# Kernel optimization log

Measured on AMD Instinct MI355X. Metric: run time of the kernel, lower is better.

The kernel has to match this reference:

```python
import jax, jax.numpy as jnp
import numpy as np

EPS = 1e-5
SLOPE = 0.2


def _bn(x, g, b, m, v):
    # eval-mode BatchNorm1d over channel dim (last axis here)
    return (x - m) * (g * jax.lax.rsqrt(v + EPS)) + b


def _lrelu(x):
    return jnp.where(x >= 0, x, SLOPE * x)


def setup_inputs() -> dict:
    key = jax.random.key(0)
    ks = jax.random.split(key, 24)
    B, N = 16, 2048
    d = {
        "x_query": jax.random.normal(ks[0], (B, 2048), jnp.float32),
        "x_key": jax.random.normal(ks[1], (B, N, 512), jnp.float32),
        "W1": jax.random.normal(ks[2], (2048, 512), jnp.float32) * 0.02,
        "W2": jax.random.normal(ks[3], (512, 2048), jnp.float32) * 0.02,
        "W3": jax.random.normal(ks[4], (64, 512), jnp.float32) * 0.02,
        "W4": jax.random.normal(ks[5], (1, 64), jnp.float32) * 0.02,
    }
    for i, c in zip(range(4), (2048, 512, 64, 1)):
        d[f"g{i+1}"] = jax.random.uniform(ks[6 + 4 * i], (c,), jnp.float32, 0.5, 1.5)
        d[f"b{i+1}"] = jax.random.normal(ks[7 + 4 * i], (c,), jnp.float32) * 0.1
        d[f"m{i+1}"] = jax.random.normal(ks[8 + 4 * i], (c,), jnp.float32) * 0.1
        d[f"v{i+1}"] = jax.random.uniform(ks[9 + 4 * i], (c,), jnp.float32, 0.5, 1.5)
    return d


def reference(x_query, x_key, W1, W2, W3, W4,
              g1, b1, m1, v1, g2, b2, m2, v2,
              g3, b3, m3, v3, g4, b4, m4, v4):
    # values: [B, N, 2048]
    values = _lrelu(_bn(jnp.einsum('bnd,ed->bne', x_key, W1), g1, b1, m1, v1))
    features = values + x_query[:, None, :]
    s = _lrelu(_bn(jnp.einsum('bne,de->bnd', features, W2), g2, b2, m2, v2))
    s = _lrelu(_bn(jnp.einsum('bnd,kd->bnk', s, W3), g3, b3, m3, v3))
    s = _lrelu(_bn(jnp.einsum('bnk,ok->bno', s, W4), g4, b4, m4, v4))  # [B,N,1]
    scores = jax.nn.softmax(s[..., 0], axis=1)  # [B,N]
    feature = jnp.einsum('bne,bn->be', values, scores)  # softmax-weighted sum pool
    return feature
```

## Files before the change

### kernel.cpp

```cpp
#include <hip/hip_runtime.h>
#include <hip/hip_bf16.h>

typedef __bf16 bf16x8 __attribute__((ext_vector_type(8)));
typedef float f32x4 __attribute__((ext_vector_type(4)));
typedef __attribute__((address_space(3))) void lds_void_t;
typedef __attribute__((address_space(1))) void gbl_void_t;

#define LRELU(x) ((x) >= 0.f ? (x) : 0.2f * (x))

__device__ __forceinline__ void gload16(void* lds_uniform, const void* gsrc) {
    __builtin_amdgcn_global_load_lds((const gbl_void_t*)gsrc, (lds_void_t*)lds_uniform,
                                     16, 0, 0);
}

__device__ __forceinline__ unsigned short f2u(float f) {
    __hip_bfloat16 h = __float2bfloat16(f);
    return reinterpret_cast<unsigned short&>(h);
}

__global__ void cvt_f32_bf16(const float* __restrict__ in,
                             __hip_bfloat16* __restrict__ out, int n4) {
    int stride = gridDim.x * blockDim.x;
    for (int i = blockIdx.x * blockDim.x + threadIdx.x; i < n4; i += stride) {
        float4 v = reinterpret_cast<const float4*>(in)[i];
        ushort4 o;
        o.x = f2u(v.x); o.y = f2u(v.y); o.z = f2u(v.z); o.w = f2u(v.w);
        reinterpret_cast<ushort4*>(out)[i] = o;
    }
}

template <int N, int K, int MODE>
__global__ __launch_bounds__(512, 2)
void gemm256(const __hip_bfloat16* __restrict__ A,
             const __hip_bfloat16* __restrict__ Bw,
             const float* __restrict__ xq,
             __hip_bfloat16* __restrict__ out,
             const float* __restrict__ Gg, const float* __restrict__ Gb,
             const float* __restrict__ Gm, const float* __restrict__ Gv) {
    __shared__ __hip_bfloat16 sm[3 * 16384];

    const int nwg = gridDim.x;
    const int cpx = nwg >> 3;
    const int bid = blockIdx.x;
    const int orig = (bid & 7) * cpx + (bid >> 3);
    constexpr int NCB = N / 256;
    const int rowblk = orig / NCB;
    const int colblk = orig % NCB;
    const int row0 = rowblk * 256, col0 = colblk * 256;

    const int tid = threadIdx.x;
    const int lane = tid & 63;
    const int wv = tid >> 6;
    const int wm = wv >> 2, wn = wv & 3;
    const int lr = lane & 15, kg = lane >> 4;

    const int srow = tid >> 2;
    const int sc = tid & 3;
    const int kch = ((sc ^ ((srow >> 1) & 3)) << 3);
    const __hip_bfloat16* As0 = A + (size_t)(row0 + srow) * K + kch;
    const __hip_bfloat16* As1 = A + (size_t)(row0 + 128 + srow) * K + kch;
    const __hip_bfloat16* Bs0 = Bw + (size_t)(col0 + srow) * K + kch;
    const __hip_bfloat16* Bs1 = Bw + (size_t)(col0 + 128 + srow) * K + kch;

    auto STAGE_A = [&](int b, int k0) {
        __hip_bfloat16* la = sm + b * 16384 + wv * 512;
        gload16(la,        As0 + k0);
        gload16(la + 4096, As1 + k0);
    };
    auto STAGE_B = [&](int b, int k0) {
        __hip_bfloat16* lb = sm + b * 16384 + 8192 + wv * 512;
        gload16(lb,        Bs0 + k0);
        gload16(lb + 4096, Bs1 + k0);
    };

    const int f = (lr >> 1) & 3;
    const int koff = ((kg ^ f) << 3);
    const int aoff = (wm * 128 + lr) * 32 + koff;
    const int boff = 8192 + (wn * 64 + lr) * 32 + koff;

    f32x4 acc[8][4];
#pragma unroll
    for (int i = 0; i < 8; ++i)
#pragma unroll
        for (int j = 0; j < 4; ++j) acc[i][j] = (f32x4){0.f, 0.f, 0.f, 0.f};

    constexpr int nt = K / 32;
    STAGE_A(0, 0);  STAGE_B(0, 0);
    STAGE_A(1, 32); STAGE_B(1, 32);

    for (int t = 0; t < nt; ++t) {
        if (t + 1 < nt) {
            asm volatile("s_waitcnt vmcnt(4)" ::: "memory");
        } else {
            asm volatile("s_waitcnt vmcnt(0)" ::: "memory");
        }
        __builtin_amdgcn_s_barrier();
        __builtin_amdgcn_sched_barrier(0);

        const __hip_bfloat16* base = sm + (t % 3) * 16384;
        bf16x8 af[8], bfr[4];

        if (t + 2 < nt) {
            STAGE_A((t + 2) % 3, (t + 2) * 32);
            STAGE_B((t + 2) % 3, (t + 2) * 32);
        }
#pragma unroll
        for (int i = 0; i < 8; ++i)
            af[i] = *reinterpret_cast<const bf16x8*>(base + aoff + i * 512);
#pragma unroll
        for (int j = 0; j < 4; ++j)
            bfr[j] = *reinterpret_cast<const bf16x8*>(base + boff + j * 512);

#pragma unroll
        for (int i = 0; i < 8; ++i)
#pragma unroll
            for (int j = 0; j < 4; ++j)
                acc[i][j] = __builtin_amdgcn_mfma_f32_16x16x32_bf16(af[i], bfr[j], acc[i][j], 0, 0, 0);
    }

    const int bq = row0 >> 11;
    float scl[4], tcn[4], xqv[4];
#pragma unroll
    for (int j = 0; j < 4; ++j) {
        const int c = col0 + wn * 64 + j * 16 + lr;
        scl[j] = Gg[c] * rsqrtf(Gv[c] + 1e-5f);
        tcn[j] = Gb[c] - Gm[c] * scl[j];
        xqv[j] = (MODE == 1) ? xq[bq * 2048 + c] : 0.f;
    }
#pragma unroll
    for (int i = 0; i < 8; ++i) {
#pragma unroll
        for (int rI = 0; rI < 4; ++rI) {
            const int r = row0 + wm * 128 + i * 16 + kg * 4 + rI;
            const size_t rowoff = (size_t)r * N + col0 + wn * 64 + lr;
#pragma unroll
            for (int j = 0; j < 4; ++j) {
                float val = acc[i][j][rI] * scl[j] + tcn[j];
                val = LRELU(val) + xqv[j];
                out[rowoff + j * 16] = __float2bfloat16(val);
            }
        }
    }
}

__global__ __launch_bounds__(256)
void gemm3_l4(const __hip_bfloat16* __restrict__ A,
              const __hip_bfloat16* __restrict__ W3b,
              const float* __restrict__ W4,
              const float* __restrict__ g3, const float* __restrict__ b3,
              const float* __restrict__ m3, const float* __restrict__ v3,
              const float* __restrict__ g4, const float* __restrict__ b4,
              const float* __restrict__ m4, const float* __restrict__ v4,
              float* __restrict__ logits) {
    const int lane = threadIdx.x & 63;
    const int wv = threadIdx.x >> 6;
    const int row0 = blockIdx.x * 128 + wv * 32;
    const int lr = lane & 15, kg = lane >> 4;

    f32x4 acc[2][4];
#pragma unroll
    for (int i = 0; i < 2; ++i)
#pragma unroll
        for (int j = 0; j < 4; ++j) acc[i][j] = (f32x4){0.f, 0.f, 0.f, 0.f};

    for (int k = 0; k < 512; k += 32) {
        const int kk = k + kg * 8;
        bf16x8 a[2], b[4];
#pragma unroll
        for (int i = 0; i < 2; ++i)
            a[i] = *reinterpret_cast<const bf16x8*>(A + (size_t)(row0 + i * 16 + lr) * 512 + kk);
#pragma unroll
        for (int j = 0; j < 4; ++j)
            b[j] = *reinterpret_cast<const bf16x8*>(W3b + (size_t)(j * 16 + lr) * 512 + kk);
#pragma unroll
        for (int i = 0; i < 2; ++i)
#pragma unroll
            for (int j = 0; j < 4; ++j)
                acc[i][j] = __builtin_amdgcn_mfma_f32_16x16x32_bf16(a[i], b[j], acc[i][j], 0, 0, 0);
    }

    const float sc4 = g4[0] * rsqrtf(v4[0] + 1e-5f);
    const float tc4 = b4[0] - m4[0] * sc4;
#pragma unroll
    for (int i = 0; i < 2; ++i) {
        float t[4] = {0.f, 0.f, 0.f, 0.f};
#pragma unroll
        for (int j = 0; j < 4; ++j) {
            const int c = j * 16 + lr;
            const float sc = g3[c] * rsqrtf(v3[c] + 1e-5f);
            const float tc = b3[c] - m3[c] * sc;
            const float w4c = W4[c];
#pragma unroll
            for (int rI = 0; rI < 4; ++rI) {
                float v = acc[i][j][rI] * sc + tc;
                t[rI] += LRELU(v) * w4c;
            }
        }
#pragma unroll
        for (int m = 1; m < 16; m <<= 1)
#pragma unroll
            for (int rI = 0; rI < 4; ++rI) t[rI] += __shfl_xor(t[rI], m, 64);
        if (lr == 0) {
#pragma unroll
            for (int rI = 0; rI < 4; ++rI) {
                float lg = t[rI] * sc4 + tc4;
                logits[row0 + i * 16 + kg * 4 + rI] = LRELU(lg);
            }
        }
    }
}

__global__ void softmax2048(const float* __restrict__ logits, float* __restrict__ scores) {
    __shared__ float sh[2048];
    __shared__ float red[256];
    const int b = blockIdx.x, tid = threadIdx.x;
    float lmax = -1e30f;
#pragma unroll
    for (int it = 0; it < 8; ++it) {
        const int n = tid + it * 256;
        float v = logits[b * 2048 + n];
        sh[n] = v;
        lmax = fmaxf(lmax, v);
    }
    red[tid] = lmax;
    __syncthreads();
    for (int s = 128; s > 0; s >>= 1) {
        if (tid < s) red[tid] = fmaxf(red[tid], red[tid + s]);
        __syncthreads();
    }
    const float gmax = red[0];
    __syncthreads();
    float lsum = 0.f;
#pragma unroll
    for (int it = 0; it < 8; ++it) {
        const int n = tid + it * 256;
        float e = expf(sh[n] - gmax);
        sh[n] = e;
        lsum += e;
    }
    red[tid] = lsum;
    __syncthreads();
    for (int s = 128; s > 0; s >>= 1) {
        if (tid < s) red[tid] += red[tid + s];
        __syncthreads();
    }
    const float inv = 1.f / red[0];
#pragma unroll
    for (int it = 0; it < 8; ++it) {
        const int n = tid + it * 256;
        scores[b * 2048 + n] = sh[n] * inv;
    }
}

__global__ void pool_partial(const __hip_bfloat16* __restrict__ feats,
                             const float* __restrict__ scores,
                             float* __restrict__ partial) {
    const int b = blockIdx.y, nc = blockIdx.x;
    const int e0 = threadIdx.x * 8;
    float acc[8] = {0, 0, 0, 0, 0, 0, 0, 0};
    const size_t base = ((size_t)b * 2048 + nc * 64) * 2048;
    for (int i = 0; i < 64; ++i) {
        const float sc = scores[b * 2048 + nc * 64 + i];
        bf16x8 v = *reinterpret_cast<const bf16x8*>(feats + base + (size_t)i * 2048 + e0);
#pragma unroll
        for (int j = 0; j < 8; ++j) acc[j] += sc * (float)v[j];
    }
    float* p = partial + ((size_t)(b * 32 + nc)) * 2048 + e0;
#pragma unroll
    for (int j = 0; j < 8; ++j) p[j] = acc[j];
}

__global__ void pool_reduce(const float* __restrict__ partial,
                            const float* __restrict__ xq,
                            float* __restrict__ out) {
    const int i = blockIdx.x * blockDim.x + threadIdx.x;
    const int b = i >> 11, e = i & 2047;
    float s = 0.f;
#pragma unroll
    for (int nc = 0; nc < 32; ++nc) s += partial[((size_t)(b * 32 + nc)) * 2048 + e];
    out[i] = s - xq[i];
}

extern "C" void kernel_launch(void* const* d_in, const int* in_sizes, int n_in,
                              void* d_out, int out_size, void* d_ws, size_t ws_size,
                              hipStream_t stream) {
    const float* xq = (const float*)d_in[0];
    const float* xk = (const float*)d_in[1];
    const float* W1 = (const float*)d_in[2];
    const float* W2 = (const float*)d_in[3];
    const float* W3 = (const float*)d_in[4];
    const float* W4 = (const float*)d_in[5];
    const float* g1 = (const float*)d_in[6], *b1 = (const float*)d_in[7];
    const float* m1 = (const float*)d_in[8], *v1 = (const float*)d_in[9];
    const float* g2 = (const float*)d_in[10], *b2 = (const float*)d_in[11];
    const float* m2 = (const float*)d_in[12], *v2 = (const float*)d_in[13];
    const float* g3 = (const float*)d_in[14], *b3 = (const float*)d_in[15];
    const float* m3 = (const float*)d_in[16], *v3 = (const float*)d_in[17];
    const float* g4 = (const float*)d_in[18], *b4 = (const float*)d_in[19];
    const float* m4 = (const float*)d_in[20], *v4 = (const float*)d_in[21];

    const int M = 32768;

    char* ws = (char*)d_ws;
    size_t off = 0;
    auto alloc = [&](size_t bytes) {
        void* p = ws + off;
        off += (bytes + 255) & ~(size_t)255;
        return p;
    };
    __hip_bfloat16* xkb   = (__hip_bfloat16*)alloc((size_t)M * 512 * 2);
    __hip_bfloat16* w1b   = (__hip_bfloat16*)alloc((size_t)2048 * 512 * 2);
    __hip_bfloat16* w2b   = (__hip_bfloat16*)alloc((size_t)512 * 2048 * 2);
    __hip_bfloat16* w3b   = (__hip_bfloat16*)alloc((size_t)64 * 512 * 2);
    __hip_bfloat16* featb = (__hip_bfloat16*)alloc((size_t)M * 2048 * 2);
    __hip_bfloat16* s2b   = (__hip_bfloat16*)alloc((size_t)M * 512 * 2);
    float* logits         = (float*)alloc((size_t)M * 4);
    float* scores         = (float*)alloc((size_t)16 * 2048 * 4);
    float* partial        = (float*)alloc((size_t)16 * 32 * 2048 * 4);

    cvt_f32_bf16<<<4096, 256, 0, stream>>>(xk, xkb, M * 512 / 4);
    cvt_f32_bf16<<<1024, 256, 0, stream>>>(W1, w1b, 2048 * 512 / 4);
    cvt_f32_bf16<<<1024, 256, 0, stream>>>(W2, w2b, 512 * 2048 / 4);
    cvt_f32_bf16<<<32, 256, 0, stream>>>(W3, w3b, 64 * 512 / 4);

    gemm256<2048, 512, 1><<<1024, 512, 0, stream>>>(
        xkb, w1b, xq, featb, g1, b1, m1, v1);

    gemm256<512, 2048, 2><<<256, 512, 0, stream>>>(
        featb, w2b, nullptr, s2b, g2, b2, m2, v2);

    gemm3_l4<<<256, 256, 0, stream>>>(s2b, w3b, W4,
                                      g3, b3, m3, v3, g4, b4, m4, v4, logits);

    softmax2048<<<16, 256, 0, stream>>>(logits, scores);

    pool_partial<<<dim3(32, 16), 256, 0, stream>>>(featb, scores, partial);
    pool_reduce<<<128, 256, 0, stream>>>(partial, xq, (float*)d_out);
}
```

Before: 221.5 us.

## Rewrite GEMM mainloop as 8-phase ping-pong schedule with 64-wide K tiles

Replaces the triple-buffered K=32 mainloop with a double-buffered K=64 scheme that splits each tile into quarter sub-blocks. Global-to-LDS staging is interleaved across eight barrier-separated MFMA phases, and s_setprio raises priority during the math phases. The LDS swizzle is changed to a 64-wide XOR pattern and occupancy drops to one workgroup per CU because LDS use is larger. The aim is to hide load latency and LDS reads behind MFMA within a single workgroup, at the cost of many more barriers and lower occupancy.

```diff
diff --git a/kernel.cpp b/kernel.cpp
--- a/kernel.cpp
+++ b/kernel.cpp
@@ -29,24 +29,74 @@
     }
 }
 
+
+#define MMQ(AF, BF, IH, JH)                                                   \
+    {                                                                         \
+        _Pragma("unroll") for (int r = 0; r < 4; ++r) {                       \
+            _Pragma("unroll") for (int c = 0; c < 2; ++c) {                   \
+                _Pragma("unroll") for (int s = 0; s < 2; ++s) {               \
+                    acc[(IH) * 4 + r][(JH) * 2 + c] =                         \
+                        __builtin_amdgcn_mfma_f32_16x16x32_bf16(              \
+                            AF[r][s], BF[c][s],                               \
+                            acc[(IH) * 4 + r][(JH) * 2 + c], 0, 0, 0);        \
+                }                                                             \
+            }                                                                 \
+        }                                                                     \
+    }
+
+#define LDA_(AF, BUF, IH)                                                     \
+    {                                                                         \
+        const __hip_bfloat16* _ab = sm + (BUF) * 32768 + wm * 8192;           \
+        _Pragma("unroll") for (int r = 0; r < 4; ++r) {                       \
+            const int _row = (IH) * 64 + r * 16 + lr;                         \
+            _Pragma("unroll") for (int s = 0; s < 2; ++s) {                   \
+                AF[r][s] = *reinterpret_cast<const bf16x8*>(                  \
+                    _ab + _row * 64 + (((s * 4 + kg) ^ (lr & 7)) * 8));       \
+            }                                                                 \
+        }                                                                     \
+    }
+
+#define LDB_(BF, BUF, JH)                                                     \
+    {                                                                         \
+        const __hip_bfloat16* _bb =                                           \
+            sm + (BUF) * 32768 + (2 + (wn >> 1)) * 8192;                      \
+        _Pragma("unroll") for (int c = 0; c < 2; ++c) {                       \
+            const int _row = (wn & 1) * 64 + ((JH) * 2 + c) * 16 + lr;        \
+            _Pragma("unroll") for (int s = 0; s < 2; ++s) {                   \
+                BF[c][s] = *reinterpret_cast<const bf16x8*>(                  \
+                    _bb + _row * 64 + (((s * 4 + kg) ^ (lr & 7)) * 8));       \
+            }                                                                 \
+        }                                                                     \
+    }
+
+#define PH_MID                                                                \
+    __builtin_amdgcn_s_barrier();                                             \
+    asm volatile("s_waitcnt lgkmcnt(0)" ::: "memory");                        \
+    __builtin_amdgcn_sched_barrier(0);                                        \
+    __builtin_amdgcn_s_setprio(1);
+
+#define PH_END                                                                \
+    __builtin_amdgcn_s_setprio(0);                                            \
+    __builtin_amdgcn_sched_barrier(0);                                        \
+    __builtin_amdgcn_s_barrier();
+
 template <int N, int K, int MODE>
-__global__ __launch_bounds__(512, 2)
-void gemm256(const __hip_bfloat16* __restrict__ A,
-             const __hip_bfloat16* __restrict__ Bw,
-             const float* __restrict__ xq,
-             __hip_bfloat16* __restrict__ out,
-             const float* __restrict__ Gg, const float* __restrict__ Gb,
-             const float* __restrict__ Gm, const float* __restrict__ Gv) {
-    __shared__ __hip_bfloat16 sm[3 * 16384];
+__global__ __launch_bounds__(512, 1)
+void gemm8p(const __hip_bfloat16* __restrict__ A,
+            const __hip_bfloat16* __restrict__ Bw,
+            const float* __restrict__ xq,
+            __hip_bfloat16* __restrict__ out,
+            const float* __restrict__ Gg, const float* __restrict__ Gb,
+            const float* __restrict__ Gm, const float* __restrict__ Gv) {
+    __shared__ __hip_bfloat16 sm[65536];
 
     const int nwg = gridDim.x;
     const int cpx = nwg >> 3;
     const int bid = blockIdx.x;
     const int orig = (bid & 7) * cpx + (bid >> 3);
     constexpr int NCB = N / 256;
-    const int rowblk = orig / NCB;
-    const int colblk = orig % NCB;
-    const int row0 = rowblk * 256, col0 = colblk * 256;
+    const int row0 = (orig / NCB) * 256;
+    const int col0 = (orig % NCB) * 256;
 
     const int tid = threadIdx.x;
     const int lane = tid & 63;
@@ -54,29 +104,16 @@
     const int wm = wv >> 2, wn = wv & 3;
     const int lr = lane & 15, kg = lane >> 4;
 
-    const int srow = tid >> 2;
-    const int sc = tid & 3;
-    const int kch = ((sc ^ ((srow >> 1) & 3)) << 3);
-    const __hip_bfloat16* As0 = A + (size_t)(row0 + srow) * K + kch;
-    const __hip_bfloat16* As1 = A + (size_t)(row0 + 128 + srow) * K + kch;
-    const __hip_bfloat16* Bs0 = Bw + (size_t)(col0 + srow) * K + kch;
-    const __hip_bfloat16* Bs1 = Bw + (size_t)(col0 + 128 + srow) * K + kch;
-
-    auto STAGE_A = [&](int b, int k0) {
-        __hip_bfloat16* la = sm + b * 16384 + wv * 512;
-        gload16(la,        As0 + k0);
-        gload16(la + 4096, As1 + k0);
+    const int schunk = (tid & 7) ^ ((tid >> 3) & 7);
+    const __hip_bfloat16* srcA0 = A + (size_t)(row0 + (tid >> 3)) * K + schunk * 8;
+    const __hip_bfloat16* srcB0 = Bw + (size_t)(col0 + (tid >> 3)) * K + schunk * 8;
+    constexpr size_t H = (size_t)128 * K;
+
+    auto STG = [&](int buf, int region, const __hip_bfloat16* src) {
+        __hip_bfloat16* l = sm + buf * 32768 + region * 8192 + wv * 512;
+        gload16(l, src);
+        gload16(l + 4096, src + (size_t)64 * K);
     };
-    auto STAGE_B = [&](int b, int k0) {
-        __hip_bfloat16* lb = sm + b * 16384 + 8192 + wv * 512;
-        gload16(lb,        Bs0 + k0);
-        gload16(lb + 4096, Bs1 + k0);
-    };
-
-    const int f = (lr >> 1) & 3;
-    const int koff = ((kg ^ f) << 3);
-    const int aoff = (wm * 128 + lr) * 32 + koff;
-    const int boff = 8192 + (wn * 64 + lr) * 32 + koff;
 
     f32x4 acc[8][4];
 #pragma unroll
@@ -84,38 +121,63 @@
 #pragma unroll
         for (int j = 0; j < 4; ++j) acc[i][j] = (f32x4){0.f, 0.f, 0.f, 0.f};
 
-    constexpr int nt = K / 32;
-    STAGE_A(0, 0);  STAGE_B(0, 0);
-    STAGE_A(1, 32); STAGE_B(1, 32);
-
-    for (int t = 0; t < nt; ++t) {
-        if (t + 1 < nt) {
+    bf16x8 af[4][2], bfrL[2][2], bfrH[2][2];
+
+    STG(0, 0, srcA0);
+    STG(0, 1, srcA0 + H);
+    STG(0, 2, srcB0);
+    STG(0, 3, srcB0 + H);
+    STG(1, 2, srcB0 + 64);
+    STG(1, 3, srcB0 + H + 64);
+    asm volatile("s_waitcnt vmcnt(4)" ::: "memory");
+    __builtin_amdgcn_s_barrier();
+
+    constexpr int niter = K / 128;
+    for (int it = 0; it < niter; ++it) {
+        const int k0 = it * 128;
+        const bool pf = (it + 1 < niter);
+
+        LDA_(af, 0, 0);
+        LDB_(bfrL, 0, 0);
+        STG(1, 0, srcA0 + k0 + 64);
+        PH_MID; MMQ(af, bfrL, 0, 0); PH_END;
+
+        LDB_(bfrH, 0, 1);
+        STG(1, 1, srcA0 + H + k0 + 64);
+        PH_MID; MMQ(af, bfrH, 0, 1); PH_END;
+
+        LDA_(af, 0, 1);
+        if (pf) STG(0, 2, srcB0 + k0 + 128);
+        PH_MID; MMQ(af, bfrH, 1, 1); PH_END;
+
+        if (pf) {
+            STG(0, 3, srcB0 + H + k0 + 128);
             asm volatile("s_waitcnt vmcnt(4)" ::: "memory");
         } else {
             asm volatile("s_waitcnt vmcnt(0)" ::: "memory");
         }
-        __builtin_amdgcn_s_barrier();
-        __builtin_amdgcn_sched_barrier(0);
-
-        const __hip_bfloat16* base = sm + (t % 3) * 16384;
-        bf16x8 af[8], bfr[4];
-
-        if (t + 2 < nt) {
-            STAGE_A((t + 2) % 3, (t + 2) * 32);
-            STAGE_B((t + 2) % 3, (t + 2) * 32);
+        PH_MID; MMQ(af, bfrL, 1, 0); PH_END;
+
+        LDA_(af, 1, 0);
+        LDB_(bfrL, 1, 0);
+        if (pf) STG(0, 0, srcA0 + k0 + 128);
+        PH_MID; MMQ(af, bfrL, 0, 0); PH_END;
+
+        LDB_(bfrH, 1, 1);
+        if (pf) STG(0, 1, srcA0 + H + k0 + 128);
+        PH_MID; MMQ(af, bfrH, 0, 1); PH_END;
+
+        LDA_(af, 1, 1);
+        if (pf) STG(1, 2, srcB0 + k0 + 192);
+        PH_MID; MMQ(af, bfrH, 1, 1); PH_END;
+
+        if (pf) {
+            STG(1, 3, srcB0 + H + k0 + 192);
+            asm volatile("s_waitcnt vmcnt(4)" ::: "memory");
+        } else {
+            asm volatile("s_waitcnt vmcnt(0)" ::: "memory");
         }
-#pragma unroll
-        for (int i = 0; i < 8; ++i)
-            af[i] = *reinterpret_cast<const bf16x8*>(base + aoff + i * 512);
-#pragma unroll
-        for (int j = 0; j < 4; ++j)
-            bfr[j] = *reinterpret_cast<const bf16x8*>(base + boff + j * 512);
-
-#pragma unroll
-        for (int i = 0; i < 8; ++i)
-#pragma unroll
-            for (int j = 0; j < 4; ++j)
-                acc[i][j] = __builtin_amdgcn_mfma_f32_16x16x32_bf16(af[i], bfr[j], acc[i][j], 0, 0, 0);
+        PH_MID; MMQ(af, bfrL, 1, 0); PH_END;
     }
 
     const int bq = row0 >> 11;
@@ -323,10 +385,10 @@
     cvt_f32_bf16<<<1024, 256, 0, stream>>>(W2, w2b, 512 * 2048 / 4);
     cvt_f32_bf16<<<32, 256, 0, stream>>>(W3, w3b, 64 * 512 / 4);
 
-    gemm256<2048, 512, 1><<<1024, 512, 0, stream>>>(
+    gemm8p<2048, 512, 1><<<1024, 512, 0, stream>>>(
         xkb, w1b, xq, featb, g1, b1, m1, v1);
 
-    gemm256<512, 2048, 2><<<256, 512, 0, stream>>>(
+    gemm8p<512, 2048, 2><<<256, 512, 0, stream>>>(
         featb, w2b, nullptr, s2b, g2, b2, m2, v2);
 
     gemm3_l4<<<256, 256, 0, stream>>>(s2b, w3b, W4,
```

New measurement: 214.7 us. 3.1% less time.

## Deepen GEMM LDS pipeline to four buffers with split-phase MFMA scheduling

Applied to the files above, without the earlier changes.

The main GEMM kernel moves from a 3-stage to a 4-stage LDS ring. Each K-step is split into two half-tiles, with staged A and B loads interleaved between MFMA phases, barriers between them, and s_setprio raising wave priority around the MFMA blocks. Launch bounds drop to one block per SM to fit the larger 128KB shared buffer. The four fp32-to-bf16 conversion launches are also merged into one kernel. This trades occupancy and extra barriers for deeper latency hiding and fewer launches.

```diff
diff --git a/kernel.cpp b/kernel.cpp
--- a/kernel.cpp
+++ b/kernel.cpp
@@ -18,35 +18,48 @@
     return reinterpret_cast<unsigned short&>(h);
 }
 
-__global__ void cvt_f32_bf16(const float* __restrict__ in,
-                             __hip_bfloat16* __restrict__ out, int n4) {
-    int stride = gridDim.x * blockDim.x;
-    for (int i = blockIdx.x * blockDim.x + threadIdx.x; i < n4; i += stride) {
-        float4 v = reinterpret_cast<const float4*>(in)[i];
-        ushort4 o;
-        o.x = f2u(v.x); o.y = f2u(v.y); o.z = f2u(v.z); o.w = f2u(v.w);
-        reinterpret_cast<ushort4*>(out)[i] = o;
+__global__ void cvt_fused(const float* __restrict__ a, __hip_bfloat16* __restrict__ oa, int na,
+                          const float* __restrict__ b, __hip_bfloat16* __restrict__ ob, int nb,
+                          const float* __restrict__ c, __hip_bfloat16* __restrict__ oc, int nc,
+                          const float* __restrict__ d, __hip_bfloat16* __restrict__ od, int nd) {
+    const int stride = gridDim.x * blockDim.x;
+    const int total = na + nb + nc + nd;
+    for (int i = blockIdx.x * blockDim.x + threadIdx.x; i < total; i += stride) {
+        const float* s; __hip_bfloat16* o; int j = i;
+        if (j < na) { s = a; o = oa; }
+        else {
+            j -= na;
+            if (j < nb) { s = b; o = ob; }
+            else {
+                j -= nb;
+                if (j < nc) { s = c; o = oc; }
+                else { j -= nc; s = d; o = od; }
+            }
+        }
+        float4 v = reinterpret_cast<const float4*>(s)[j];
+        ushort4 u;
+        u.x = f2u(v.x); u.y = f2u(v.y); u.z = f2u(v.z); u.w = f2u(v.w);
+        reinterpret_cast<ushort4*>(o)[j] = u;
     }
 }
 
 template <int N, int K, int MODE>
-__global__ __launch_bounds__(512, 2)
-void gemm256(const __hip_bfloat16* __restrict__ A,
-             const __hip_bfloat16* __restrict__ Bw,
-             const float* __restrict__ xq,
-             __hip_bfloat16* __restrict__ out,
-             const float* __restrict__ Gg, const float* __restrict__ Gb,
-             const float* __restrict__ Gm, const float* __restrict__ Gv) {
-    __shared__ __hip_bfloat16 sm[3 * 16384];
+__global__ __launch_bounds__(512, 1)
+void gemm4b(const __hip_bfloat16* __restrict__ A,
+            const __hip_bfloat16* __restrict__ Bw,
+            const float* __restrict__ xq,
+            __hip_bfloat16* __restrict__ out,
+            const float* __restrict__ Gg, const float* __restrict__ Gb,
+            const float* __restrict__ Gm, const float* __restrict__ Gv) {
+    __shared__ __hip_bfloat16 sm[4 * 16384];
 
     const int nwg = gridDim.x;
     const int cpx = nwg >> 3;
     const int bid = blockIdx.x;
     const int orig = (bid & 7) * cpx + (bid >> 3);
     constexpr int NCB = N / 256;
-    const int rowblk = orig / NCB;
-    const int colblk = orig % NCB;
-    const int row0 = rowblk * 256, col0 = colblk * 256;
+    const int row0 = (orig / NCB) * 256;
+    const int col0 = (orig % NCB) * 256;
 
     const int tid = threadIdx.x;
     const int lane = tid & 63;
@@ -84,38 +97,60 @@
 #pragma unroll
         for (int j = 0; j < 4; ++j) acc[i][j] = (f32x4){0.f, 0.f, 0.f, 0.f};
 
-    constexpr int nt = K / 32;
+    constexpr int niter = K / 32;
     STAGE_A(0, 0);  STAGE_B(0, 0);
     STAGE_A(1, 32); STAGE_B(1, 32);
-
-    for (int t = 0; t < nt; ++t) {
-        if (t + 1 < nt) {
+    STAGE_A(2, 64); STAGE_B(2, 64);
+    asm volatile("s_waitcnt vmcnt(8)" ::: "memory");
+    __builtin_amdgcn_s_barrier();
+
+    for (int t = 0; t < niter; ++t) {
+        const __hip_bfloat16* base = sm + (t & 3) * 16384;
+        bf16x8 af[4], bf[4];
+
+        if (t + 3 < niter) STAGE_A((t + 3) & 3, (t + 3) * 32);
+#pragma unroll
+        for (int i = 0; i < 4; ++i)
+            af[i] = *reinterpret_cast<const bf16x8*>(base + aoff + i * 512);
+#pragma unroll
+        for (int j = 0; j < 4; ++j)
+            bf[j] = *reinterpret_cast<const bf16x8*>(base + boff + j * 512);
+        __builtin_amdgcn_s_barrier();
+        asm volatile("s_waitcnt lgkmcnt(0)" ::: "memory");
+        __builtin_amdgcn_sched_barrier(0);
+        __builtin_amdgcn_s_setprio(1);
+#pragma unroll
+        for (int i = 0; i < 4; ++i)
+#pragma unroll
+            for (int j = 0; j < 4; ++j)
+                acc[i][j] = __builtin_amdgcn_mfma_f32_16x16x32_bf16(af[i], bf[j], acc[i][j], 0, 0, 0);
+        __builtin_amdgcn_s_setprio(0);
+        __builtin_amdgcn_sched_barrier(0);
+        __builtin_amdgcn_s_barrier();
+
+        if (t + 3 < niter) {
+            STAGE_B((t + 3) & 3, (t + 3) * 32);
+            asm volatile("s_waitcnt vmcnt(8)" ::: "memory");
+        } else if (t + 2 < niter) {
             asm volatile("s_waitcnt vmcnt(4)" ::: "memory");
         } else {
             asm volatile("s_waitcnt vmcnt(0)" ::: "memory");
         }
+#pragma unroll
+        for (int i = 0; i < 4; ++i)
+            af[i] = *reinterpret_cast<const bf16x8*>(base + aoff + (4 + i) * 512);
         __builtin_amdgcn_s_barrier();
+        asm volatile("s_waitcnt lgkmcnt(0)" ::: "memory");
         __builtin_amdgcn_sched_barrier(0);
-
-        const __hip_bfloat16* base = sm + (t % 3) * 16384;
-        bf16x8 af[8], bfr[4];
-
-        if (t + 2 < nt) {
-            STAGE_A((t + 2) % 3, (t + 2) * 32);
-            STAGE_B((t + 2) % 3, (t + 2) * 32);
-        }
-#pragma unroll
-        for (int i = 0; i < 8; ++i)
-            af[i] = *reinterpret_cast<const bf16x8*>(base + aoff + i * 512);
-#pragma unroll
-        for (int j = 0; j < 4; ++j)
-            bfr[j] = *reinterpret_cast<const bf16x8*>(base + boff + j * 512);
-
-#pragma unroll
-        for (int i = 0; i < 8; ++i)
+        __builtin_amdgcn_s_setprio(1);
+#pragma unroll
+        for (int i = 0; i < 4; ++i)
 #pragma unroll
             for (int j = 0; j < 4; ++j)
-                acc[i][j] = __builtin_amdgcn_mfma_f32_16x16x32_bf16(af[i], bfr[j], acc[i][j], 0, 0, 0);
+                acc[4 + i][j] = __builtin_amdgcn_mfma_f32_16x16x32_bf16(af[i], bf[j], acc[4 + i][j], 0, 0, 0);
+        __builtin_amdgcn_s_setprio(0);
+        __builtin_amdgcn_sched_barrier(0);
+        __builtin_amdgcn_s_barrier();
     }
 
     const int bq = row0 >> 11;
@@ -318,15 +353,16 @@
     float* scores         = (float*)alloc((size_t)16 * 2048 * 4);
     float* partial        = (float*)alloc((size_t)16 * 32 * 2048 * 4);
 
-    cvt_f32_bf16<<<4096, 256, 0, stream>>>(xk, xkb, M * 512 / 4);
-    cvt_f32_bf16<<<1024, 256, 0, stream>>>(W1, w1b, 2048 * 512 / 4);
-    cvt_f32_bf16<<<1024, 256, 0, stream>>>(W2, w2b, 512 * 2048 / 4);
-    cvt_f32_bf16<<<32, 256, 0, stream>>>(W3, w3b, 64 * 512 / 4);
-
-    gemm256<2048, 512, 1><<<1024, 512, 0, stream>>>(
+    cvt_fused<<<4096, 256, 0, stream>>>(
+        xk, xkb, M * 512 / 4,
+        W1, w1b, 2048 * 512 / 4,
+        W2, w2b, 512 * 2048 / 4,
+        W3, w3b, 64 * 512 / 4);
+
+    gemm4b<2048, 512, 1><<<1024, 512, 0, stream>>>(
         xkb, w1b, xq, featb, g1, b1, m1, v1);
 
-    gemm256<512, 2048, 2><<<256, 512, 0, stream>>>(
+    gemm4b<512, 2048, 2><<<256, 512, 0, stream>>>(
         featb, w2b, nullptr, s2b, g2, b2, m2, v2);
 
     gemm3_l4<<<256, 256, 0, stream>>>(s2b, w3b, W4,
```

Result: no change. 224.4 us (+1.3%).
